# Kernel optimization log

Measured on AMD Instinct MI355X. Metric: run time of the kernel, lower is better.

The kernel has to match this reference:

```python
import jax, jax.numpy as jnp
import numpy as np

NUM_SINK = 8   # cfg.SINKHORN_ITERS
MASS = 0.9     # marginal value used for a and b


def _graph_conv(x, W_enc, b_enc, W1, b1, W2, b2, k):
    # Node encoder
    h = jax.nn.relu(x @ W_enc + b_enc)                       # [G,M,D]
    # kNN in embedding space (per graph)
    sq = jnp.sum(h * h, axis=-1)                             # [G,M]
    d2 = sq[:, :, None] + sq[:, None, :] - 2.0 * jnp.einsum('gmd,gnd->gmn', h, h)
    d2 = d2 + jnp.eye(h.shape[1], dtype=h.dtype) * 1e9       # exclude self-loop
    _, idx = jax.lax.top_k(-d2, k)                           # [G,M,k]
    neigh = jax.vmap(lambda hg, ig: hg[ig])(h, idx)          # [G,M,k,D]
    hc = jnp.broadcast_to(h[:, :, None, :], neigh.shape)
    e = jnp.concatenate([hc, neigh - hc], axis=-1)           # [G,M,k,2D]
    e = jax.nn.relu(e @ W1 + b1)                             # edge embed
    e = e @ W2 + b2                                          # back to D
    return jnp.max(e, axis=2)                                # max-aggregate over neighbors


def _sinkhorn(cost, lam):
    # log-domain unrolled Sinkhorn, batched over graphs; a=b=0.9 marginals
    log_p = -cost / lam                                      # [G,M,N]
    log_m = jnp.log(jnp.asarray(MASS, cost.dtype))
    for _ in range(NUM_SINK - 1):
        log_p = log_p - (jax.nn.logsumexp(log_p, axis=2, keepdims=True) - log_m)
        log_p = log_p - (jax.nn.logsumexp(log_p, axis=1, keepdims=True) - log_m)
    log_p = log_p - (jax.nn.logsumexp(log_p, axis=2, keepdims=True) - log_m)
    return jnp.exp(log_p)


def setup_inputs() -> dict:
    key = jax.random.key(0)
    ks = jax.random.split(key, 6)
    G, M, D = 64, 256, 256
    E = 256  # edge embed size
    inp = {
        'tra_x': jax.random.normal(ks[0], (G, M, D), jnp.float32),
        'det_x': jax.random.normal(ks[1], (G, M, D), jnp.float32),
        'W_enc': jax.random.normal(ks[2], (D, D), jnp.float32) / np.sqrt(D),
        'b_enc': jnp.zeros((D,), jnp.float32),
        'W1': jax.random.normal(ks[3], (2 * D, E), jnp.float32) / np.sqrt(2 * D),
        'b1': jnp.zeros((E,), jnp.float32),
        'W2': jax.random.normal(ks[4], (E, D), jnp.float32) / np.sqrt(E),
        'b2': jnp.zeros((D,), jnp.float32),
        'eplison': jnp.zeros((1,), jnp.float32),
        'k': 16,
    }
    return inp


def reference(tra_x, det_x, W_enc, b_enc, W1, b1, W2, b2, eplison, k):
    tra = _graph_conv(tra_x, W_enc, b_enc, W1, b1, W2, b2, k)  # [G,M,D]
    det = _graph_conv(det_x, W_enc, b_enc, W1, b1, W2, b2, k)  # [G,N,D]
    corr = jnp.einsum('gmd,gnd->gmn', tra, det)
    n1 = jnp.linalg.norm(tra, axis=-1)                         # [G,M]
    n2 = jnp.linalg.norm(det, axis=-1)                         # [G,N]
    cost = -corr / (n1[:, :, None] * n2[:, None, :])
    lam = jnp.exp(eplison[0]) + 0.03
    return _sinkhorn(cost, lam)                                # [G,M,N]
```

## Files before the change

kernel.cpp:

```cpp
#include <hip/hip_runtime.h>
#include <math.h>

#define NG 64
#define NM 256
#define ND 256
#define NK 16
#define NR (NG * NM)
#define NB 32

#define MASSF 0.9f

typedef _Float16 f16;
typedef __attribute__((ext_vector_type(8))) _Float16 f16x8;
typedef __attribute__((ext_vector_type(4))) _Float16 f16x4;
typedef __attribute__((ext_vector_type(4))) float f32x4;
typedef __attribute__((ext_vector_type(4))) unsigned u32x4;

static __device__ __forceinline__ unsigned pkrelu(unsigned a, unsigned b) {
  unsigned r;
  asm("v_pk_add_f16 %0, %1, %2" : "=v"(r) : "v"(a), "v"(b));
  asm("v_pk_max_f16 %0, %1, %2" : "=v"(r) : "v"(r), "v"(0u));
  return r;
}

__global__ __launch_bounds__(256) void prep_k(const float* __restrict__ W1,
                                              const float* __restrict__ b1,
                                              const float* __restrict__ W2,
                                              f16* __restrict__ w2t, f16* __restrict__ w1cat,
                                              float* __restrict__ biascat) {
  const int b = blockIdx.x, k = threadIdx.x;
  if (b < 256) {
    w2t[b * 256 + k] = (f16)W2[(size_t)k * 256 + b];
  } else {
    const int n = b - 256;
    float v;
    if (n < 256)
      v = W1[(size_t)k * 256 + n] - W1[(size_t)(k + 256) * 256 + n];
    else
      v = W1[(size_t)(k + 256) * 256 + (n - 256)];
    w1cat[(size_t)n * 256 + k] = (f16)v;
    if (k == 0) biascat[n] = (n < 256) ? b1[n] : 0.f;
  }
}

__global__ __launch_bounds__(256) void gemm_nn2m_k(const float* __restrict__ A0,
                                                   const float* __restrict__ A1,
                                                   const float* __restrict__ B,
                                                   const float* __restrict__ bias,
                                                   float* __restrict__ h2) {
  __shared__ float As[2][16][68];
  __shared__ float Bs[2][16][128];
  const int tid = threadIdx.x;
  const int tx = tid & 15, ty = tid >> 4;
  const int half = blockIdx.y >> 8;
  const int m0 = (blockIdx.y & 255) * 64, n0 = blockIdx.x * 128;
  const float* A = half ? A1 : A0;
  float* C = h2 + (size_t)half * NR * ND;
  const int arow = tid >> 2, akc = (tid & 3) * 4;
  const int bkr = tid >> 4, bcc = (tid & 15) * 4;
  float4 av, bv0, bv1;
  float acc[4][8] = {};
  auto gload = [&](int k0) {
    av = *(const float4*)&A[(size_t)(m0 + arow) * 256 + k0 + akc];
    bv0 = *(const float4*)&B[(size_t)(k0 + bkr) * 256 + n0 + bcc];
    bv1 = *(const float4*)&B[(size_t)(k0 + bkr) * 256 + n0 + 64 + bcc];
  };
  auto swrite = [&](int buf) {
    As[buf][akc + 0][arow] = av.x;
    As[buf][akc + 1][arow] = av.y;
    As[buf][akc + 2][arow] = av.z;
    As[buf][akc + 3][arow] = av.w;
    *(float4*)&Bs[buf][bkr][bcc] = bv0;
    *(float4*)&Bs[buf][bkr][64 + bcc] = bv1;
  };
  gload(0);
  swrite(0);
  __syncthreads();
  for (int s = 0; s < 16; ++s) {
    if (s < 15) gload((s + 1) * 16);
    const int buf = s & 1;
#pragma unroll
    for (int kk = 0; kk < 16; ++kk) {
      const float4 a0 = *(const float4*)&As[buf][kk][ty * 4];
      const float4 b0 = *(const float4*)&Bs[buf][kk][tx * 4];
      const float4 b1 = *(const float4*)&Bs[buf][kk][64 + tx * 4];
      const float aa[4] = {a0.x, a0.y, a0.z, a0.w};
      const float bb[8] = {b0.x, b0.y, b0.z, b0.w, b1.x, b1.y, b1.z, b1.w};
#pragma unroll
      for (int i = 0; i < 4; ++i)
#pragma unroll
        for (int j = 0; j < 8; ++j) acc[i][j] = fmaf(aa[i], bb[j], acc[i][j]);
    }
    if (s < 15) swrite((s + 1) & 1);
    __syncthreads();
  }
  const float4 bia0 = *(const float4*)&bias[n0 + tx * 4];
  const float4 bia1 = *(const float4*)&bias[n0 + 64 + tx * 4];
#pragma unroll
  for (int i = 0; i < 4; ++i) {
    const size_t row = (size_t)(m0 + ty * 4 + i);
    float4 o0 = {fmaxf(acc[i][0] + bia0.x, 0.f), fmaxf(acc[i][1] + bia0.y, 0.f),
                 fmaxf(acc[i][2] + bia0.z, 0.f), fmaxf(acc[i][3] + bia0.w, 0.f)};
    float4 o1 = {fmaxf(acc[i][4] + bia1.x, 0.f), fmaxf(acc[i][5] + bia1.y, 0.f),
                 fmaxf(acc[i][6] + bia1.z, 0.f), fmaxf(acc[i][7] + bia1.w, 0.f)};
    *(float4*)&C[row * 256 + n0 + tx * 4] = o0;
    *(float4*)&C[row * 256 + n0 + 64 + tx * 4] = o1;
  }
}

__global__ __launch_bounds__(256) void gemm_nt2m_k(const float* __restrict__ h2,
                                                   float* __restrict__ S0,
                                                   float* __restrict__ S1,
                                                   float* __restrict__ sq2) {
  const int flat0 = blockIdx.x;
  const int flat = ((flat0 & 7) << 7) | (flat0 >> 3);
  const int half = flat >> 9;
  const int inner = flat & 511;
  const int bx = inner & 1, by = (inner >> 1) & 3, g = inner >> 3;
  if (bx == 0 && by >= 2) return;
  __shared__ float As[2][16][68];
  __shared__ float Bs[2][16][128];
  const float* Ag = h2 + (size_t)half * NR * ND + (size_t)g * NM * ND;
  float* Cg = (half ? S1 : S0) + (size_t)g * NM * NM;
  float* sq = sq2 + half * NR + g * 256;
  const int tid = threadIdx.x;
  const int tx = tid & 15, ty = tid >> 4;
  const int m0 = by * 64, n0 = bx * 128;
  const int arow = tid >> 2, akc = (tid & 3) * 4;
  const int brow = tid >> 1, bkc = (tid & 1) * 8;
  float4 av, bva, bvb;
  float acc[4][8] = {};
  auto gload = [&](int k0) {
    av = *(const float4*)&Ag[(size_t)(m0 + arow) * 256 + k0 + akc];
    bva = *(const float4*)&Ag[(size_t)(n0 + brow) * 256 + k0 + bkc];
    bvb = *(const float4*)&Ag[(size_t)(n0 + brow) * 256 + k0 + bkc + 4];
  };
  auto swrite = [&](int buf) {
    As[buf][akc + 0][arow] = av.x;
    As[buf][akc + 1][arow] = av.y;
    As[buf][akc + 2][arow] = av.z;
    As[buf][akc + 3][arow] = av.w;
    Bs[buf][bkc + 0][brow] = bva.x;
    Bs[buf][bkc + 1][brow] = bva.y;
    Bs[buf][bkc + 2][brow] = bva.z;
    Bs[buf][bkc + 3][brow] = bva.w;
    Bs[buf][bkc + 4][brow] = bvb.x;
    Bs[buf][bkc + 5][brow] = bvb.y;
    Bs[buf][bkc + 6][brow] = bvb.z;
    Bs[buf][bkc + 7][brow] = bvb.w;
  };
  gload(0);
  swrite(0);
  __syncthreads();
  for (int s = 0; s < 16; ++s) {
    if (s < 15) gload((s + 1) * 16);
    const int buf = s & 1;
#pragma unroll
    for (int kk = 0; kk < 16; ++kk) {
      const float4 a0 = *(const float4*)&As[buf][kk][ty * 4];
      const float4 b0 = *(const float4*)&Bs[buf][kk][tx * 4];
      const float4 b1 = *(const float4*)&Bs[buf][kk][64 + tx * 4];
      const float aa[4] = {a0.x, a0.y, a0.z, a0.w};
      const float bb[8] = {b0.x, b0.y, b0.z, b0.w, b1.x, b1.y, b1.z, b1.w};
#pragma unroll
      for (int i = 0; i < 4; ++i)
#pragma unroll
        for (int j = 0; j < 8; ++j) acc[i][j] = fmaf(aa[i], bb[j], acc[i][j]);
    }
    if (s < 15) swrite((s + 1) & 1);
    __syncthreads();
  }
  const int c0 = n0 + tx * 4, c1 = n0 + 64 + tx * 4;
#pragma unroll
  for (int i = 0; i < 4; ++i) {
    const int row = m0 + ty * 4 + i;
    float4 o0 = {acc[i][0], acc[i][1], acc[i][2], acc[i][3]};
    float4 o1 = {acc[i][4], acc[i][5], acc[i][6], acc[i][7]};
    *(float4*)&Cg[(size_t)row * 256 + c0] = o0;
    *(float4*)&Cg[(size_t)row * 256 + c1] = o1;
    if (row >= c0 && row < c0 + 4) sq[row] = acc[i][row - c0];
    if (row >= c1 && row < c1 + 4) sq[row] = acc[i][4 + row - c1];
  }
  if (bx == 1 && by < 2) {
#pragma unroll
    for (int j = 0; j < 4; ++j) {
      const size_t col0 = (size_t)(n0 + tx * 4 + j);
      const size_t col1 = (size_t)(n0 + 64 + tx * 4 + j);
      float4 t0 = {acc[0][j], acc[1][j], acc[2][j], acc[3][j]};
      float4 t1 = {acc[0][4 + j], acc[1][4 + j], acc[2][4 + j], acc[3][4 + j]};
      *(float4*)&Cg[col0 * 256 + m0 + ty * 4] = t0;
      *(float4*)&Cg[col1 * 256 + m0 + ty * 4] = t1;
    }
  }
}

__global__ __launch_bounds__(256, 2) void mlp1m_mfma_k(const float* __restrict__ h2,
                                                       const f16* __restrict__ Bt,
                                                       const float* __restrict__ biascat,
                                                       f16* __restrict__ baseb2,
                                                       f16* __restrict__ n1b2) {
  __shared__ char As[64 * 512];
  const int tid = threadIdx.x;
  const int l = tid & 63, wv = tid >> 6;
  const int r = l & 15, gq = l >> 4;
  const int half = blockIdx.y >> 8;
  const int m0 = (blockIdx.y & 255) * 64, n0 = blockIdx.x * 128;
  const float* A = h2 + (size_t)half * NR * ND;
  f16x8 bfr[2][8];
  float bv[2];
#pragma unroll
  for (int nt = 0; nt < 2; ++nt) {
    const int col = n0 + wv * 32 + nt * 16 + r;
    const f16* wb = Bt + (size_t)col * 256 + gq * 8;
#pragma unroll
    for (int ks = 0; ks < 8; ++ks) bfr[nt][ks] = *(const f16x8*)(wb + ks * 32);
    bv[nt] = biascat[col];
  }
  const int row = tid >> 2, ch = tid & 3;
  const float* ag = A + (size_t)(m0 + row) * 256 + ch * 64;
  char* lb = As + row * 512;
#pragma unroll
  for (int j = 0; j < 8; ++j) {
    const float4 x0 = *(const float4*)(ag + j * 8);
    const float4 x1 = *(const float4*)(ag + j * 8 + 4);
    f16x8 w = {(f16)x0.x, (f16)x0.y, (f16)x0.z, (f16)x0.w,
               (f16)x1.x, (f16)x1.y, (f16)x1.z, (f16)x1.w};
    *(f16x8*)(lb + (((ch * 128 + j * 16)) ^ ((row & 7) << 4))) = w;
  }
  __syncthreads();
  f32x4 acc[4][2];
#pragma unroll
  for (int mt = 0; mt < 4; ++mt)
#pragma unroll
    for (int nt = 0; nt < 2; ++nt) acc[mt][nt] = (f32x4){0.f, 0.f, 0.f, 0.f};
#pragma unroll
  for (int ks = 0; ks < 8; ++ks) {
    f16x8 a[4];
#pragma unroll
    for (int mt = 0; mt < 4; ++mt)
      a[mt] = *(const f16x8*)(As + (mt * 16 + r) * 512 + ((gq * 16 + ks * 64) ^ ((r & 7) << 4)));
#pragma unroll
    for (int mt = 0; mt < 4; ++mt)
#pragma unroll
      for (int nt = 0; nt < 2; ++nt)
        acc[mt][nt] = __builtin_amdgcn_mfma_f32_16x16x32_f16(a[mt], bfr[nt][ks], acc[mt][nt], 0, 0, 0);
  }
  f16* dst = ((n0 < 256) ? baseb2 : n1b2) + (size_t)half * NR * ND;
  const int cb = (n0 < 256) ? n0 : n0 - 256;
#pragma unroll
  for (int mt = 0; mt < 4; ++mt)
#pragma unroll
    for (int nt = 0; nt < 2; ++nt) {
      const int col = cb + wv * 32 + nt * 16 + r;
#pragma unroll
      for (int reg = 0; reg < 4; ++reg) {
        const int rw = m0 + mt * 16 + gq * 4 + reg;
        dst[(size_t)rw * 256 + col] = (f16)(acc[mt][nt][reg] + bv[nt]);
      }
    }
}

__global__ __launch_bounds__(256, 2) void cost_mfma_k(const f16* __restrict__ featT,
                                                      const f16* __restrict__ featD,
                                                      const float* __restrict__ nA,
                                                      const float* __restrict__ nB,
                                                      const float* __restrict__ eps,
                                                      float* __restrict__ P) {
  __shared__ char As[64 * 512];
  const int flat = ((blockIdx.x & 7) << 6) | (blockIdx.x >> 3);
  const int bx = flat & 1, by = (flat >> 1) & 3, g = flat >> 3;
  const f16* A = featT + (size_t)g * NM * ND;
  const f16* Bt = featD + (size_t)g * NM * ND;
  const int tid = threadIdx.x;
  const int l = tid & 63, wv = tid >> 6;
  const int r = l & 15, gq = l >> 4;
  const int m0 = by * 64, n0 = bx * 128;
  f16x8 bfr[2][8];
  float rnb[2];
#pragma unroll
  for (int nt = 0; nt < 2; ++nt) {
    const int col = n0 + wv * 32 + nt * 16 + r;
    const f16* wb = Bt + (size_t)col * 256 + gq * 8;
#pragma unroll
    for (int ks = 0; ks < 8; ++ks) bfr[nt][ks] = *(const f16x8*)(wb + ks * 32);
    rnb[nt] = 1.0f / nB[g * NM + col];
  }
  const int row = tid >> 2, ch = tid & 3;
  const char* ag = (const char*)(A + (size_t)(m0 + row) * 256) + ch * 128;
  char* lb = As + row * 512;
#pragma unroll
  for (int j = 0; j < 8; ++j)
    *(f16x8*)(lb + (((ch * 128 + j * 16)) ^ ((row & 7) << 4))) = *(const f16x8*)(ag + j * 16);
  __syncthreads();
  f32x4 acc[4][2];
#pragma unroll
  for (int mt = 0; mt < 4; ++mt)
#pragma unroll
    for (int nt = 0; nt < 2; ++nt) acc[mt][nt] = (f32x4){0.f, 0.f, 0.f, 0.f};
#pragma unroll
  for (int ks = 0; ks < 8; ++ks) {
    f16x8 a[4];
#pragma unroll
    for (int mt = 0; mt < 4; ++mt)
      a[mt] = *(const f16x8*)(As + (mt * 16 + r) * 512 + ((gq * 16 + ks * 64) ^ ((r & 7) << 4)));
#pragma unroll
    for (int mt = 0; mt < 4; ++mt)
#pragma unroll
      for (int nt = 0; nt < 2; ++nt)
        acc[mt][nt] = __builtin_amdgcn_mfma_f32_16x16x32_f16(a[mt], bfr[nt][ks], acc[mt][nt], 0, 0, 0);
  }
  const float inv_lam = 1.0f / (expf(eps[0]) + 0.03f);
#pragma unroll
  for (int mt = 0; mt < 4; ++mt) {
    float ria[4];
#pragma unroll
    for (int reg = 0; reg < 4; ++reg)
      ria[reg] = inv_lam / nA[g * NM + m0 + mt * 16 + gq * 4 + reg];
#pragma unroll
    for (int nt = 0; nt < 2; ++nt) {
      const int col = n0 + wv * 32 + nt * 16 + r;
#pragma unroll
      for (int reg = 0; reg < 4; ++reg) {
        const int rw = m0 + mt * 16 + gq * 4 + reg;
        P[(size_t)g * NM * NM + (size_t)rw * 256 + col] =
            expf(acc[mt][nt][reg] * ria[reg] * rnb[nt]);
      }
    }
  }
}

__global__ __launch_bounds__(256) void topk2_k(const float* __restrict__ S0,
                                               const float* __restrict__ S1,
                                               const float* __restrict__ sq2,
                                               int* __restrict__ idx2) {
  const int w = threadIdx.x >> 6, lane = threadIdx.x & 63;
  const int x = blockIdx.x & 7, j = blockIdx.x >> 3;
  const int half = x >> 2;
  const int g = ((x & 3) << 4) + (j >> 6);
  const int lrow = g * 256 + (j & 63) * 4 + w;
  const int m = lrow & 255;
  const float* Srow = (half ? S1 : S0) + (size_t)lrow * NM;
  const float* sqg = sq2 + half * NR + g * NM;
  int* idx = idx2 + (size_t)half * NR * NK;
  const float sm = sqg[m];
  const float4 sv = *(const float4*)&Srow[lane * 4];
  const float4 qv = *(const float4*)&sqg[lane * 4];
  float cand[4] = {sm + qv.x - 2.f * sv.x, sm + qv.y - 2.f * sv.y, sm + qv.z - 2.f * sv.z,
                   sm + qv.w - 2.f * sv.w};
#pragma unroll
  for (int t = 0; t < 4; ++t)
    if (lane * 4 + t == m) cand[t] = 1e30f;
  for (int rnd = 0; rnd < NK; ++rnd) {
    float bvv = cand[0];
    int bi = lane * 4;
#pragma unroll
    for (int t = 1; t < 4; ++t)
      if (cand[t] < bvv) {
        bvv = cand[t];
        bi = lane * 4 + t;
      }
#pragma unroll
    for (int off = 1; off < 64; off <<= 1) {
      const float ov = __shfl_xor(bvv, off);
      const int oi = __shfl_xor(bi, off);
      if (ov < bvv || (ov == bvv && oi < bi)) {
        bvv = ov;
        bi = oi;
      }
    }
    if (lane == 0) idx[(size_t)lrow * NK + rnd] = bi;
    if ((bi >> 2) == lane) cand[bi & 3] = 1e30f;
  }
}

__global__ __launch_bounds__(512, 4) void edgemlp_mfma10_k(
    const f16* __restrict__ baseb2, const f16* __restrict__ n1b2, const int* __restrict__ idx2,
    const f16* __restrict__ w2t, const float* __restrict__ b2, f16* __restrict__ featf2,
    float* __restrict__ nrm2) {
  __shared__ unsigned E[2][2][512 * 4];
  __shared__ int sidx[NB * NK];
  __shared__ float normp[NB][8];
  const int tid = threadIdx.x;
  const int l = tid & 63, wv = tid >> 6;
  const size_t SZH = (size_t)NR * ND;
  const int bid = blockIdx.x;
  const int half = bid >> 9;
  const int b9 = bid & 511;
  const int blk = ((b9 & 7) << 6) | (b9 >> 3);
  const int node0 = blk * NB;
  const int g = node0 >> 8;
  const f16* baseb = baseb2 + (size_t)half * SZH;
  const f16* n1b = n1b2 + (size_t)half * SZH;
  const int* idx = idx2 + (size_t)half * NR * NK;
  f16* featf = featf2 + (size_t)half * SZH;
  float* nrm = nrm2 + (size_t)half * NR;
  const int r = l & 15, gq = l >> 4;
  sidx[tid] = idx[(size_t)node0 * NK + tid];
  f16x8 bfr[2][8];
  float b2v[2];
#pragma unroll
  for (int t = 0; t < 2; ++t) {
    const int nb = wv * 2 + t;
    const f16* wb = w2t + (size_t)(nb * 16 + r) * 256 + gq * 8;
#pragma unroll
    for (int ks = 0; ks < 8; ++ks) bfr[t][ks] = *(const f16x8*)(wb + ks * 32);
    b2v[t] = b2[nb * 16 + r];
  }
  __syncthreads();
  const int r_s = tid & 15;
  const int col_s = ((tid >> 6) * 32) + (((tid >> 4) & 3) * 8);
  u32x4 bs0, ns0, bs1, ns1;
  auto sload = [&](int s) {
    const int na = s * 2;
    bs0 = *(const u32x4*)(baseb + (((size_t)(node0 + na)) << 8) + col_s);
    ns0 = *(const u32x4*)(n1b + ((((size_t)g << 8) + sidx[na * NK + r_s]) << 8) + col_s);
    bs1 = *(const u32x4*)(baseb + (((size_t)(node0 + na + 1)) << 8) + col_s);
    ns1 = *(const u32x4*)(n1b + ((((size_t)g << 8) + sidx[(na + 1) * NK + r_s]) << 8) + col_s);
  };
  auto swrite = [&](int s) {
    const int buf = s & 1;
    u32x4 w0, w1;
#pragma unroll
    for (int q = 0; q < 4; ++q) {
      w0[q] = pkrelu(bs0[q], ns0[q]);
      w1[q] = pkrelu(bs1[q], ns1[q]);
    }
    *(u32x4*)&E[buf][0][tid * 4] = w0;
    *(u32x4*)&E[buf][1][tid * 4] = w1;
  };
  sload(0);
  swrite(0);
  __syncthreads();
  for (int s = 0; s < NB / 2; ++s) {
    if (s + 1 < NB / 2) sload(s + 1);
    const int buf = s & 1;
#pragma unroll
    for (int q = 0; q < 2; ++q) {
      const char* eb = (const char*)&E[buf][q][0];
      f32x4 acc0 = (f32x4){0.f, 0.f, 0.f, 0.f};
      f32x4 acc1 = (f32x4){0.f, 0.f, 0.f, 0.f};
#pragma unroll
      for (int ks = 0; ks < 8; ++ks) {
        const f16x8 a = *(const f16x8*)(eb + ks * 1024 + l * 16);
        acc0 = __builtin_amdgcn_mfma_f32_16x16x32_f16(a, bfr[0][ks], acc0, 0, 0, 0);
        acc1 = __builtin_amdgcn_mfma_f32_16x16x32_f16(a, bfr[1][ks], acc1, 0, 0, 0);
      }
      const int nd = node0 + s * 2 + q;
      float m0v = fmaxf(fmaxf(acc0[0], acc0[1]), fmaxf(acc0[2], acc0[3]));
      m0v = fmaxf(m0v, __shfl_xor(m0v, 16));
      m0v = fmaxf(m0v, __shfl_xor(m0v, 32));
      float m1v = fmaxf(fmaxf(acc1[0], acc1[1]), fmaxf(acc1[2], acc1[3]));
      m1v = fmaxf(m1v, __shfl_xor(m1v, 16));
      m1v = fmaxf(m1v, __shfl_xor(m1v, 32));
      const f16 h0 = (f16)(m0v + b2v[0]);
      const f16 h1 = (f16)(m1v + b2v[1]);
      if (gq == 0) {
        featf[((size_t)nd << 8) + (wv * 2 + 0) * 16 + r] = h0;
        featf[((size_t)nd << 8) + (wv * 2 + 1) * 16 + r] = h1;
      }
      const float o0 = (float)h0, o1 = (float)h1;
      float ss = o0 * o0 + o1 * o1;
      ss += __shfl_xor(ss, 1);
      ss += __shfl_xor(ss, 2);
      ss += __shfl_xor(ss, 4);
      ss += __shfl_xor(ss, 8);
      if (l == 0) normp[s * 2 + q][wv] = ss;
    }
    if (s + 1 < NB / 2) swrite(s + 1);
    __syncthreads();
  }
  if (tid < NB) {
    float s = 0.f;
#pragma unroll
    for (int w = 0; w < 8; ++w) s += normp[tid][w];
    nrm[node0 + tid] = sqrtf(s);
  }
}

__global__ __launch_bounds__(1024) void sinkhorn_k(float* __restrict__ P) {
  __shared__ float red[16][256];
  __shared__ float scal[256];
  const int t = threadIdx.x;
  const int tc = t & 15;
  const int trw = t >> 4;
  const int wv = t >> 6, l = t & 63;
  float* Pg = P + (size_t)blockIdx.x * NM * NM;
  float p[4][16];
#pragma unroll
  for (int i = 0; i < 4; ++i)
#pragma unroll
    for (int q = 0; q < 4; ++q)
      *(f32x4*)&p[i][q * 4] = *(const f32x4*)&Pg[(size_t)(trw * 4 + i) * NM + tc * 16 + q * 4];

  auto rowpass = [&]() {
#pragma unroll
    for (int i = 0; i < 4; ++i) {
      float s = p[i][0];
#pragma unroll
      for (int j = 1; j < 16; ++j) s += p[i][j];
      s += __shfl_xor(s, 1);
      s += __shfl_xor(s, 2);
      s += __shfl_xor(s, 4);
      s += __shfl_xor(s, 8);
      const float sc = MASSF / s;
#pragma unroll
      for (int j = 0; j < 16; ++j) p[i][j] *= sc;
    }
  };
  auto colpass = [&]() {
    float tmp[16];
#pragma unroll
    for (int j = 0; j < 16; ++j) tmp[j] = ((p[0][j] + p[1][j]) + (p[2][j] + p[3][j]));
#pragma unroll
    for (int j = 0; j < 16; ++j) {
      tmp[j] += __shfl_xor(tmp[j], 16);
      tmp[j] += __shfl_xor(tmp[j], 32);
    }
    if (l < 16) {
#pragma unroll
      for (int q = 0; q < 4; ++q)
        *(f32x4*)&red[wv][l * 16 + q * 4] = *(const f32x4*)&tmp[q * 4];
    }
    __syncthreads();
    if (t < 256) {
      float s = red[0][t];
#pragma unroll
      for (int w = 1; w < 16; ++w) s += red[w][t];
      scal[t] = MASSF / s;
    }
    __syncthreads();
#pragma unroll
    for (int j = 0; j < 16; ++j) {
      const float sc = scal[tc * 16 + j];
#pragma unroll
      for (int i = 0; i < 4; ++i) p[i][j] *= sc;
    }
    __syncthreads();
  };
  for (int it = 0; it < 7; ++it) {
    rowpass();
    colpass();
  }
  rowpass();
#pragma unroll
  for (int i = 0; i < 4; ++i)
#pragma unroll
    for (int q = 0; q < 4; ++q)
      *(f32x4*)&Pg[(size_t)(trw * 4 + i) * NM + tc * 16 + q * 4] = *(const f32x4*)&p[i][q * 4];
}

extern "C" void kernel_launch(void* const* d_in, const int* in_sizes, int n_in, void* d_out,
                              int out_size, void* d_ws, size_t ws_size, hipStream_t stream) {
  const float* tra_x = (const float*)d_in[0];
  const float* det_x = (const float*)d_in[1];
  const float* W_enc = (const float*)d_in[2];
  const float* b_enc = (const float*)d_in[3];
  const float* W1 = (const float*)d_in[4];
  const float* b1 = (const float*)d_in[5];
  const float* W2 = (const float*)d_in[6];
  const float* b2 = (const float*)d_in[7];
  const float* eps = (const float*)d_in[8];
  float* out = (float*)d_out;

  const size_t SZ = (size_t)NR * ND;
  float* h2 = (float*)d_ws;
  f16* baseb = (f16*)(h2 + 2 * SZ);
  f16* n1b = baseb + 2 * SZ;
  f16* featT = n1b + 2 * SZ;
  f16* featD = featT + SZ;
  float* S1 = (float*)featT;
  float* sq2 = (float*)(featD + SZ);
  float* nT = sq2 + 2 * NR;
  float* nD = nT + NR;
  int* idx = (int*)(nD + NR);
  f16* w2t = (f16*)(idx + 2 * (size_t)NR * NK);
  f16* w1cat = w2t + 256 * 256;
  float* biascat = (float*)(w1cat + 512 * 256);
  float* S0 = out;

  prep_k<<<768, 256, 0, stream>>>(W1, b1, W2, w2t, w1cat, biascat);
  gemm_nn2m_k<<<dim3(2, 512), 256, 0, stream>>>(tra_x, det_x, W_enc, b_enc, h2);
  mlp1m_mfma_k<<<dim3(4, 512), 256, 0, stream>>>(h2, w1cat, biascat, baseb, n1b);
  gemm_nt2m_k<<<1024, 256, 0, stream>>>(h2, S0, S1, sq2);
  topk2_k<<<8192, 256, 0, stream>>>(S0, S1, sq2, idx);
  edgemlp_mfma10_k<<<1024, 512, 0, stream>>>(baseb, n1b, idx, w2t, b2, featT, nT);
  cost_mfma_k<<<512, 256, 0, stream>>>(featT, featD, nT, nD, eps, out);
  sinkhorn_k<<<NG, 1024, 0, stream>>>(out);
}
```

Baseline: 355.0 us.

## Restructure edge MLP so each wave holds its nodes' edge tiles in registers

The edge-MLP kernel used to stage gathered, ReLU'd edge features through double-buffered shared memory, with each wave holding two output-column tiles of W2. Now each wave owns four nodes and keeps their full 16x256 edge tiles in registers as MFMA A-operands. It streams all 16 column tiles of W2 from global/L2 and needs no shared memory or block barriers. This removes LDS traffic and syncs, but each wave now re-reads the whole W2, register pressure rises (128 VGPRs of A fragments), and the occupancy hint is dropped.

Result: slower. 465.5 us (+31.1%).

```diff
diff --git a/kernel.cpp b/kernel.cpp
--- a/kernel.cpp
+++ b/kernel.cpp
@@ -373,13 +373,10 @@
   }
 }
 
-__global__ __launch_bounds__(512, 4) void edgemlp_mfma10_k(
+__global__ __launch_bounds__(512) void edgemlp_mfma11_k(
     const f16* __restrict__ baseb2, const f16* __restrict__ n1b2, const int* __restrict__ idx2,
     const f16* __restrict__ w2t, const float* __restrict__ b2, f16* __restrict__ featf2,
     float* __restrict__ nrm2) {
-  __shared__ unsigned E[2][2][512 * 4];
-  __shared__ int sidx[NB * NK];
-  __shared__ float normp[NB][8];
   const int tid = threadIdx.x;
   const int l = tid & 63, wv = tid >> 6;
   const size_t SZH = (size_t)NR * ND;
@@ -387,93 +384,65 @@
   const int half = bid >> 9;
   const int b9 = bid & 511;
   const int blk = ((b9 & 7) << 6) | (b9 >> 3);
-  const int node0 = blk * NB;
-  const int g = node0 >> 8;
+  const int node0 = blk * NB + wv * 4;
+  const int g = (blk * NB) >> 8;
   const f16* baseb = baseb2 + (size_t)half * SZH;
   const f16* n1b = n1b2 + (size_t)half * SZH;
   const int* idx = idx2 + (size_t)half * NR * NK;
   f16* featf = featf2 + (size_t)half * SZH;
   float* nrm = nrm2 + (size_t)half * NR;
   const int r = l & 15, gq = l >> 4;
-  sidx[tid] = idx[(size_t)node0 * NK + tid];
-  f16x8 bfr[2][8];
-  float b2v[2];
-#pragma unroll
-  for (int t = 0; t < 2; ++t) {
-    const int nb = wv * 2 + t;
+  union u2h {
+    u32x4 u;
+    f16x8 h;
+  };
+  f16x8 afr[4][8];
+#pragma unroll
+  for (int n = 0; n < 4; ++n) {
+    const int nd = node0 + n;
+    const int nbr = idx[(size_t)nd * NK + r];
+    const f16* bp = baseb + ((size_t)nd << 8);
+    const f16* np = n1b + ((size_t)(g * NM + nbr) << 8);
+#pragma unroll
+    for (int ks = 0; ks < 8; ++ks) {
+      const int c = ks * 32 + gq * 8;
+      const u32x4 bv = *(const u32x4*)(bp + c);
+      const u32x4 nv = *(const u32x4*)(np + c);
+      u2h w;
+#pragma unroll
+      for (int q = 0; q < 4; ++q) w.u[q] = pkrelu(bv[q], nv[q]);
+      afr[n][ks] = w.h;
+    }
+  }
+  float ssn[4] = {0.f, 0.f, 0.f, 0.f};
+  for (int nb = 0; nb < 16; ++nb) {
+    f16x8 bfr[8];
     const f16* wb = w2t + (size_t)(nb * 16 + r) * 256 + gq * 8;
 #pragma unroll
-    for (int ks = 0; ks < 8; ++ks) bfr[t][ks] = *(const f16x8*)(wb + ks * 32);
-    b2v[t] = b2[nb * 16 + r];
-  }
-  __syncthreads();
-  const int r_s = tid & 15;
-  const int col_s = ((tid >> 6) * 32) + (((tid >> 4) & 3) * 8);
-  u32x4 bs0, ns0, bs1, ns1;
-  auto sload = [&](int s) {
-    const int na = s * 2;
-    bs0 = *(const u32x4*)(baseb + (((size_t)(node0 + na)) << 8) + col_s);
-    ns0 = *(const u32x4*)(n1b + ((((size_t)g << 8) + sidx[na * NK + r_s]) << 8) + col_s);
-    bs1 = *(const u32x4*)(baseb + (((size_t)(node0 + na + 1)) << 8) + col_s);
-    ns1 = *(const u32x4*)(n1b + ((((size_t)g << 8) + sidx[(na + 1) * NK + r_s]) << 8) + col_s);
-  };
-  auto swrite = [&](int s) {
-    const int buf = s & 1;
-    u32x4 w0, w1;
-#pragma unroll
-    for (int q = 0; q < 4; ++q) {
-      w0[q] = pkrelu(bs0[q], ns0[q]);
-      w1[q] = pkrelu(bs1[q], ns1[q]);
-    }
-    *(u32x4*)&E[buf][0][tid * 4] = w0;
-    *(u32x4*)&E[buf][1][tid * 4] = w1;
-  };
-  sload(0);
-  swrite(0);
-  __syncthreads();
-  for (int s = 0; s < NB / 2; ++s) {
-    if (s + 1 < NB / 2) sload(s + 1);
-    const int buf = s & 1;
-#pragma unroll
-    for (int q = 0; q < 2; ++q) {
-      const char* eb = (const char*)&E[buf][q][0];
-      f32x4 acc0 = (f32x4){0.f, 0.f, 0.f, 0.f};
-      f32x4 acc1 = (f32x4){0.f, 0.f, 0.f, 0.f};
-#pragma unroll
-      for (int ks = 0; ks < 8; ++ks) {
-        const f16x8 a = *(const f16x8*)(eb + ks * 1024 + l * 16);
-        acc0 = __builtin_amdgcn_mfma_f32_16x16x32_f16(a, bfr[0][ks], acc0, 0, 0, 0);
-        acc1 = __builtin_amdgcn_mfma_f32_16x16x32_f16(a, bfr[1][ks], acc1, 0, 0, 0);
-      }
-      const int nd = node0 + s * 2 + q;
-      float m0v = fmaxf(fmaxf(acc0[0], acc0[1]), fmaxf(acc0[2], acc0[3]));
-      m0v = fmaxf(m0v, __shfl_xor(m0v, 16));
-      m0v = fmaxf(m0v, __shfl_xor(m0v, 32));
-      float m1v = fmaxf(fmaxf(acc1[0], acc1[1]), fmaxf(acc1[2], acc1[3]));
-      m1v = fmaxf(m1v, __shfl_xor(m1v, 16));
-      m1v = fmaxf(m1v, __shfl_xor(m1v, 32));
-      const f16 h0 = (f16)(m0v + b2v[0]);
-      const f16 h1 = (f16)(m1v + b2v[1]);
-      if (gq == 0) {
-        featf[((size_t)nd << 8) + (wv * 2 + 0) * 16 + r] = h0;
-        featf[((size_t)nd << 8) + (wv * 2 + 1) * 16 + r] = h1;
-      }
-      const float o0 = (float)h0, o1 = (float)h1;
-      float ss = o0 * o0 + o1 * o1;
-      ss += __shfl_xor(ss, 1);
-      ss += __shfl_xor(ss, 2);
-      ss += __shfl_xor(ss, 4);
-      ss += __shfl_xor(ss, 8);
-      if (l == 0) normp[s * 2 + q][wv] = ss;
-    }
-    if (s + 1 < NB / 2) swrite(s + 1);
-    __syncthreads();
-  }
-  if (tid < NB) {
-    float s = 0.f;
-#pragma unroll
-    for (int w = 0; w < 8; ++w) s += normp[tid][w];
-    nrm[node0 + tid] = sqrtf(s);
+    for (int ks = 0; ks < 8; ++ks) bfr[ks] = *(const f16x8*)(wb + ks * 32);
+    const float b2v = b2[nb * 16 + r];
+#pragma unroll
+    for (int n = 0; n < 4; ++n) {
+      f32x4 acc = (f32x4){0.f, 0.f, 0.f, 0.f};
+#pragma unroll
+      for (int ks = 0; ks < 8; ++ks)
+        acc = __builtin_amdgcn_mfma_f32_16x16x32_f16(afr[n][ks], bfr[ks], acc, 0, 0, 0);
+      float m1 = fmaxf(fmaxf(acc[0], acc[1]), fmaxf(acc[2], acc[3]));
+      m1 = fmaxf(m1, __shfl_xor(m1, 16));
+      m1 = fmaxf(m1, __shfl_xor(m1, 32));
+      const f16 hv = (f16)(m1 + b2v);
+      if (gq == 0) featf[(((size_t)(node0 + n)) << 8) + nb * 16 + r] = hv;
+      float s2 = (float)hv * (float)hv;
+      s2 += __shfl_xor(s2, 1);
+      s2 += __shfl_xor(s2, 2);
+      s2 += __shfl_xor(s2, 4);
+      s2 += __shfl_xor(s2, 8);
+      ssn[n] += s2;
+    }
+  }
+  if (l == 0) {
+#pragma unroll
+    for (int n = 0; n < 4; ++n) nrm[node0 + n] = sqrtf(ssn[n]);
   }
 }
 
@@ -583,7 +552,7 @@
   mlp1m_mfma_k<<<dim3(4, 512), 256, 0, stream>>>(h2, w1cat, biascat, baseb, n1b);
   gemm_nt2m_k<<<1024, 256, 0, stream>>>(h2, S0, S1, sq2);
   topk2_k<<<8192, 256, 0, stream>>>(S0, S1, sq2, idx);
-  edgemlp_mfma10_k<<<1024, 512, 0, stream>>>(baseb, n1b, idx, w2t, b2, featT, nT);
+  edgemlp_mfma11_k<<<1024, 512, 0, stream>>>(baseb, n1b, idx, w2t, b2, featT, nT);
   cost_mfma_k<<<512, 256, 0, stream>>>(featT, featD, nT, nD, eps, out);
   sinkhorn_k<<<NG, 1024, 0, stream>>>(out);
 }
```
